# Kernel optimization log

Hardware: AMD Instinct MI355X
Metric: run time of the kernel (lower is better)

## Reference

```python
import jax, jax.numpy as jnp
import numpy as np

B, S, E, H, DH, W = 2, 4096, 1024, 16, 64, 512
NB = S // W          # number of query blocks
U = 2 * W            # key block = previous block + current block
INIT = 0.02


def setup_inputs() -> dict:
    key = jax.random.key(0)
    ks = jax.random.split(key, 6)
    x = jax.random.normal(ks[0], (B, S, E), jnp.float32)
    bias = jax.random.normal(ks[1], (H, W), jnp.float32)  # per-head alibi over rel. distance 0..W-1
    Wq = INIT * jax.random.normal(ks[2], (E, H, DH), jnp.float32)
    Wk = INIT * jax.random.normal(ks[3], (E, DH), jnp.float32)   # MQA: single shared K head
    Wv = INIT * jax.random.normal(ks[4], (E, DH), jnp.float32)   # MQA: single shared V head
    Wo = INIT * jax.random.normal(ks[5], (H, DH, E), jnp.float32)
    return {"x": x, "bias": bias, "Wq": Wq, "Wk": Wk, "Wv": Wv, "Wo": Wo}


def _sliding_window_attn(q, k, v, bias):
    # q: [B,S,H,DH]; k,v: [B,S,DH] (shared across heads); bias: [H,W]
    scale = 1.0 / np.sqrt(DH)
    qb = q.reshape(B, NB, W, H, DH)
    # pad one window of zeros in front so every query block sees a 'previous' block
    kp = jnp.pad(k, ((0, 0), (W, 0), (0, 0)))
    vp = jnp.pad(v, ((0, 0), (W, 0), (0, 0)))
    idx = jnp.arange(NB)[:, None] * W + jnp.arange(U)[None, :]  # [NB,U] into padded seq
    kb = kp[:, idx]  # [B,NB,U,DH]
    vb = vp[:, idx]  # [B,NB,U,DH]
    # scores over (query-in-block w, key-in-2W-block u)
    scores = jnp.einsum('bnwhd,bnud->bhnwu', qb, kb) * scale  # [B,H,NB,W,U]
    t = jnp.arange(W)
    u = jnp.arange(U)
    d = t[:, None] - u[None, :] + W                 # relative distance i-j, [W,U]
    rel_ok = (d >= 0) & (d < W)                     # causal + within window
    j_global = idx - W                              # global key position, [NB,U]
    valid = rel_ok[None, :, :] & (j_global >= 0)[:, None, :]  # [NB,W,U]
    bmat = bias[:, jnp.clip(d, 0, W - 1)]           # [H,W,U]
    scores = scores + bmat[None, :, None, :, :]
    neg = jnp.finfo(scores.dtype).min / 2
    scores = jnp.where(valid[None, None], scores, neg)
    p = jax.nn.softmax(scores, axis=-1)
    out = jnp.einsum('bhnwu,bnud->bnwhd', p, vb)    # [B,NB,W,H,DH]
    return out.reshape(B, S, H, DH)


def reference(x, bias, Wq, Wk, Wv, Wo):
    q = jnp.einsum('bse,ehd->bshd', x, Wq)
    k = jnp.einsum('bse,ed->bsd', x, Wk)
    v = jnp.einsum('bse,ed->bsd', x, Wv)
    attn = _sliding_window_attn(q, k, v, bias)
    return jnp.einsum('bshd,hde->bse', attn, Wo)
```

## Files before the change

### kernel.cpp

```cpp
#include <hip/hip_runtime.h>

#define Bx 2
#define Sx 4096
#define Ex 1024
#define Hx 16
#define DHx 64
#define Wwin 512

typedef unsigned short u16;
typedef __attribute__((ext_vector_type(8))) short bf16x8;
typedef __attribute__((ext_vector_type(4))) float f32x4;
typedef __attribute__((ext_vector_type(4))) unsigned short u16x4;

__device__ __forceinline__ u16 f2b(float f) {
  unsigned u = __builtin_bit_cast(unsigned, f);
  unsigned r = (u + 0x7FFFu + ((u >> 16) & 1u)) >> 16;
  return (u16)r;
}

__device__ __forceinline__ void gload_lds16(const void* g, void* l) {
  __builtin_amdgcn_global_load_lds(
      (const __attribute__((address_space(1))) void*)g,
      (__attribute__((address_space(3))) void*)l, 16, 0, 0);
}

__global__ __launch_bounds__(256) void cast_x_kernel(const float* __restrict__ x,
                                                     u16* __restrict__ xb) {
  long idx = ((long)blockIdx.x * 256 + threadIdx.x) * 4;
  float4 v = *(const float4*)(x + idx);
  u16x4 o;
  o[0] = f2b(v.x); o[1] = f2b(v.y); o[2] = f2b(v.z); o[3] = f2b(v.w);
  *(u16x4*)(xb + idx) = o;
}

__global__ __launch_bounds__(256) void pack_w_kernel(const float* __restrict__ Wq,
                                                     const float* __restrict__ Wk,
                                                     const float* __restrict__ Wv,
                                                     const float* __restrict__ Wo,
                                                     u16* __restrict__ wcat,
                                                     u16* __restrict__ wot) {
  int idx = blockIdx.x * 256 + threadIdx.x;
  if (idx < 1048576) {
    int e = idx >> 10, n = idx & 1023;
    wcat[n * 1024 + e] = f2b(Wq[idx]);
  } else if (idx < 1048576 + 65536) {
    int i2 = idx - 1048576;
    int e = i2 >> 6, d = i2 & 63;
    wcat[(1024 + d) * 1024 + e] = f2b(Wk[i2]);
  } else if (idx < 1048576 + 131072) {
    int i2 = idx - (1048576 + 65536);
    int e = i2 >> 6, d = i2 & 63;
    wcat[(1088 + d) * 1024 + e] = f2b(Wv[i2]);
  } else {
    int i2 = idx - (1048576 + 131072);
    int hd = i2 >> 10, e = i2 & 1023;
    wot[e * 1024 + hd] = f2b(Wo[i2]);
  }
}

template <typename OutT>
__global__ __launch_bounds__(256) void gemm_bt_kernel(const u16* __restrict__ A,
                                                      const u16* __restrict__ Bt,
                                                      OutT* __restrict__ C,
                                                      int M, int N, int K) {
  __shared__ u16 As[128 * 64];
  __shared__ u16 Bs[128 * 64];
  const int tid = threadIdx.x;
  const int lane = tid & 63, wave = tid >> 6;
  const int ll = lane & 15, gl = lane >> 4;
  const int wr = wave >> 1, wc = wave & 1;
  const long m0 = (long)blockIdx.x * 128;
  const long n0 = (long)blockIdx.y * 128;
  const int segrow = lane >> 3, cph = lane & 7;

  f32x4 acc[4][4] = {};

  for (int kb = 0; kb < K; kb += 64) {
    __syncthreads();
#pragma unroll
    for (int q = 0; q < 4; ++q) {
      int s = wave * 4 + q;
      int row = s * 8 + segrow;
      int clog = cph ^ (row & 7);
      gload_lds16(A + (m0 + row) * K + kb + clog * 8, (char*)As + s * 1024);
      gload_lds16(Bt + (n0 + row) * K + kb + clog * 8, (char*)Bs + s * 1024);
    }
    __syncthreads();
#pragma unroll
    for (int kx = 0; kx < 2; ++kx) {
      bf16x8 af[4], bfr[4];
#pragma unroll
      for (int rg = 0; rg < 4; ++rg) {
        int row = wr * 64 + rg * 16 + ll;
        int c = kx * 4 + gl;
        af[rg] = *(const bf16x8*)&As[row * 64 + ((c ^ (row & 7)) << 3)];
      }
#pragma unroll
      for (int cg = 0; cg < 4; ++cg) {
        int row = wc * 64 + cg * 16 + ll;
        int c = kx * 4 + gl;
        bfr[cg] = *(const bf16x8*)&Bs[row * 64 + ((c ^ (row & 7)) << 3)];
      }
#pragma unroll
      for (int rg = 0; rg < 4; ++rg)
#pragma unroll
        for (int cg = 0; cg < 4; ++cg)
          acc[rg][cg] = __builtin_amdgcn_mfma_f32_16x16x32_bf16(af[rg], bfr[cg],
                                                                acc[rg][cg], 0, 0, 0);
    }
  }
#pragma unroll
  for (int rg = 0; rg < 4; ++rg)
#pragma unroll
    for (int cg = 0; cg < 4; ++cg)
#pragma unroll
      for (int r = 0; r < 4; ++r) {
        long row = m0 + wr * 64 + rg * 16 + gl * 4 + r;
        long col = n0 + wc * 64 + cg * 16 + ll;
        if constexpr (sizeof(OutT) == 2)
          C[row * (long)N + col] = f2b(acc[rg][cg][r]);
        else
          C[row * (long)N + col] = acc[rg][cg][r];
      }
}

__global__ __launch_bounds__(256) void vt_transpose_kernel(const u16* __restrict__ qkvb,
                                                           u16* __restrict__ vt) {
  __shared__ u16 T[64 * 65];
  const int blk = blockIdx.x;
  const int b = blk >> 6;
  const int j0 = (blk & 63) * 64;
  const int tid = threadIdx.x;
#pragma unroll
  for (int rep = 0; rep < 16; ++rep) {
    int idx = rep * 256 + tid;
    int jj = idx >> 6, dd = idx & 63;
    T[dd * 65 + jj] = qkvb[((long)b * Sx + j0 + jj) * 1152 + 1088 + dd];
  }
  __syncthreads();
#pragma unroll
  for (int rep = 0; rep < 16; ++rep) {
    int idx = rep * 256 + tid;
    int dd = idx >> 6, jj = idx & 63;
    vt[((long)b * 64 + dd) * Sx + j0 + jj] = T[dd * 65 + jj];
  }
}

__global__ __launch_bounds__(256) void attn_kernel(const u16* __restrict__ qkv,
                                                   const u16* __restrict__ vt,
                                                   const float* __restrict__ bias,
                                                   u16* __restrict__ attnb) {
  __shared__ u16 Ks[64 * 64];
  __shared__ u16 Vts[64 * 64];
  __shared__ u16 Pb[4][32 * 64];
  __shared__ float biasS[512];

  const int bid = blockIdx.x;
  const int h = bid & 15;
  const int qt = (bid >> 4) & 31;
  const int b = bid >> 9;
  const int q0 = qt * 128;
  const long bS = (long)b * Sx;

  const int tid = threadIdx.x;
  const int lane = tid & 63, wave = tid >> 6;
  const int ll = lane & 15, gl = lane >> 4;
  const int wq0 = q0 + wave * 32;
  const int segrow = lane >> 3, cph = lane & 7;

  for (int i = tid; i < 512; i += 256) biasS[i] = bias[h * 512 + i];

  bf16x8 qf[2][2];
#pragma unroll
  for (int rg = 0; rg < 2; ++rg)
#pragma unroll
    for (int kx = 0; kx < 2; ++kx)
      qf[rg][kx] = *(const bf16x8*)&qkv[(bS + wq0 + rg * 16 + ll) * 1152 +
                                        h * 64 + kx * 32 + gl * 8];

  f32x4 oacc[2][4] = {};
  float mrow[2][4], lrow[2][4];
#pragma unroll
  for (int rg = 0; rg < 2; ++rg)
#pragma unroll
    for (int r = 0; r < 4; ++r) { mrow[rg][r] = -3e38f; lrow[rg][r] = 0.f; }

  u16* Pw = &Pb[wave][0];

  const int kb_start = (q0 - 512) > 0 ? (q0 - 512) : 0;
  const int kb_end = q0 + 64;
  for (int kb = kb_start; kb <= kb_end; kb += 64) {
#pragma unroll
    for (int q = 0; q < 2; ++q) {
      int s = wave * 2 + q;
      int rrow = s * 8 + segrow;
      int clog = cph ^ (rrow & 7);
      gload_lds16(qkv + (bS + kb + rrow) * 1152 + 1024 + clog * 8, (char*)Ks + s * 1024);
      gload_lds16(vt + ((long)b * 64 + rrow) * Sx + kb + clog * 8, (char*)Vts + s * 1024);
    }
    __syncthreads();
    const bool active = (kb <= wq0 + 31) && (kb + 63 >= wq0 - 511);
    if (active) {
      f32x4 sacc[2][4] = {};
#pragma unroll
      for (int kx = 0; kx < 2; ++kx) {
        bf16x8 kf[4];
#pragma unroll
        for (int cg = 0; cg < 4; ++cg) {
          int key = cg * 16 + ll;
          int c = kx * 4 + gl;
          kf[cg] = *(const bf16x8*)&Ks[key * 64 + ((c ^ (key & 7)) << 3)];
        }
#pragma unroll
        for (int rg = 0; rg < 2; ++rg)
#pragma unroll
          for (int cg = 0; cg < 4; ++cg)
            sacc[rg][cg] = __builtin_amdgcn_mfma_f32_16x16x32_bf16(qf[rg][kx], kf[cg],
                                                                   sacc[rg][cg], 0, 0, 0);
      }
#pragma unroll
      for (int rg = 0; rg < 2; ++rg) {
        float cmax[4] = {-3e38f, -3e38f, -3e38f, -3e38f};
#pragma unroll
        for (int cg = 0; cg < 4; ++cg)
#pragma unroll
          for (int r = 0; r < 4; ++r) {
            int i = wq0 + rg * 16 + gl * 4 + r;
            int j = kb + cg * 16 + ll;
            int d = i - j;
            int dc = d < 0 ? 0 : (d > 511 ? 511 : d);
            float sc = (d >= 0 && d < 512) ? fmaf(sacc[rg][cg][r], 0.125f, biasS[dc])
                                           : -1e30f;
            sacc[rg][cg][r] = sc;
            cmax[r] = fmaxf(cmax[r], sc);
          }
#pragma unroll
        for (int r = 0; r < 4; ++r) {
          cmax[r] = fmaxf(cmax[r], __shfl_xor(cmax[r], 1));
          cmax[r] = fmaxf(cmax[r], __shfl_xor(cmax[r], 2));
          cmax[r] = fmaxf(cmax[r], __shfl_xor(cmax[r], 4));
          cmax[r] = fmaxf(cmax[r], __shfl_xor(cmax[r], 8));
          float mnew = fmaxf(mrow[rg][r], cmax[r]);
          float f = __expf(mrow[rg][r] - mnew);
          mrow[rg][r] = mnew;
          lrow[rg][r] *= f;
#pragma unroll
          for (int cg = 0; cg < 4; ++cg) oacc[rg][cg][r] *= f;
        }
        float csum[4] = {0.f, 0.f, 0.f, 0.f};
#pragma unroll
        for (int cg = 0; cg < 4; ++cg)
#pragma unroll
          for (int r = 0; r < 4; ++r) {
            float p = __expf(sacc[rg][cg][r] - mrow[rg][r]);
            sacc[rg][cg][r] = p;
            csum[r] += p;
          }
#pragma unroll
        for (int r = 0; r < 4; ++r) {
          csum[r] += __shfl_xor(csum[r], 1);
          csum[r] += __shfl_xor(csum[r], 2);
          csum[r] += __shfl_xor(csum[r], 4);
          csum[r] += __shfl_xor(csum[r], 8);
          lrow[rg][r] += csum[r];
        }
#pragma unroll
        for (int cg = 0; cg < 4; ++cg)
#pragma unroll
          for (int r = 0; r < 4; ++r) {
            int row = rg * 16 + gl * 4 + r;
            int col = cg * 16 + ll;
            Pw[row * 64 + (((col >> 3) ^ (row & 7)) << 3) + (col & 7)] =
                f2b(sacc[rg][cg][r]);
          }
      }
#pragma unroll
      for (int kx = 0; kx < 2; ++kx) {
        bf16x8 pf[2], vf[4];
#pragma unroll
        for (int rg = 0; rg < 2; ++rg) {
          int row = rg * 16 + ll;
          int c = kx * 4 + gl;
          pf[rg] = *(const bf16x8*)&Pw[row * 64 + ((c ^ (row & 7)) << 3)];
        }
#pragma unroll
        for (int cg = 0; cg < 4; ++cg) {
          int dh = cg * 16 + ll;
          int c = kx * 4 + gl;
          vf[cg] = *(const bf16x8*)&Vts[dh * 64 + ((c ^ (dh & 7)) << 3)];
        }
#pragma unroll
        for (int rg = 0; rg < 2; ++rg)
#pragma unroll
          for (int cg = 0; cg < 4; ++cg)
            oacc[rg][cg] = __builtin_amdgcn_mfma_f32_16x16x32_bf16(pf[rg], vf[cg],
                                                                   oacc[rg][cg], 0, 0, 0);
      }
    }
    __syncthreads();
  }
#pragma unroll
  for (int rg = 0; rg < 2; ++rg)
#pragma unroll
    for (int r = 0; r < 4; ++r) {
      float inv = 1.0f / lrow[rg][r];
      long i = wq0 + rg * 16 + gl * 4 + r;
#pragma unroll
      for (int cg = 0; cg < 4; ++cg)
        attnb[(bS + i) * 1024 + h * 64 + cg * 16 + ll] = f2b(oacc[rg][cg][r] * inv);
    }
}

extern "C" void kernel_launch(void* const* d_in, const int* in_sizes, int n_in,
                              void* d_out, int out_size, void* d_ws, size_t ws_size,
                              hipStream_t stream) {
  const float* x    = (const float*)d_in[0];
  const float* bias = (const float*)d_in[1];
  const float* Wq   = (const float*)d_in[2];
  const float* Wk   = (const float*)d_in[3];
  const float* Wv   = (const float*)d_in[4];
  const float* Wo   = (const float*)d_in[5];
  float* out = (float*)d_out;

  u16* xb    = (u16*)d_ws;
  u16* wcat  = xb    + (size_t)8192 * 1024;
  u16* wot   = wcat  + (size_t)1152 * 1024;
  u16* qkvb  = wot   + (size_t)1024 * 1024;
  u16* vtb   = qkvb  + (size_t)8192 * 1152;
  u16* attnb = xb;

  cast_x_kernel<<<8192, 256, 0, stream>>>(x, xb);
  pack_w_kernel<<<8704, 256, 0, stream>>>(Wq, Wk, Wv, Wo, wcat, wot);
  gemm_bt_kernel<u16><<<dim3(64, 9), 256, 0, stream>>>(xb, wcat, qkvb, 8192, 1152, 1024);
  vt_transpose_kernel<<<128, 256, 0, stream>>>(qkvb, vtb);
  attn_kernel<<<1024, 256, 0, stream>>>(qkvb, vtb, bias, attnb);
  gemm_bt_kernel<float><<<dim3(64, 8), 256, 0, stream>>>(attnb, wot, out, 8192, 1024, 1024);
}
```

Measured before the change: 248.7 us.

## Drop online-softmax max tracking, load K/V directly per wave, compute row sums via MFMA

```diff
diff --git a/kernel.cpp b/kernel.cpp
--- a/kernel.cpp
+++ b/kernel.cpp
@@ -8,6 +8,7 @@
 #define Wwin 512
 
 typedef unsigned short u16;
+typedef unsigned int u32;
 typedef __attribute__((ext_vector_type(8))) short bf16x8;
 typedef __attribute__((ext_vector_type(4))) float f32x4;
 typedef __attribute__((ext_vector_type(4))) unsigned short u16x4;
@@ -16,6 +17,12 @@
   unsigned u = __builtin_bit_cast(unsigned, f);
   unsigned r = (u + 0x7FFFu + ((u >> 16) & 1u)) >> 16;
   return (u16)r;
+}
+
+__device__ __forceinline__ u32 cvt_pk_bf16(float lo, float hi) {
+  u32 r;
+  asm("v_cvt_pk_bf16_f32 %0, %1, %2" : "=v"(r) : "v"(lo), "v"(hi));
+  return r;
 }
 
 __device__ __forceinline__ void gload_lds16(const void* g, void* l) {
@@ -150,12 +157,11 @@
                                                    const u16* __restrict__ vt,
                                                    const float* __restrict__ bias,
                                                    u16* __restrict__ attnb) {
-  __shared__ u16 Ks[64 * 64];
-  __shared__ u16 Vts[64 * 64];
   __shared__ u16 Pb[4][32 * 64];
-  __shared__ float biasS[512];
-
-  const int bid = blockIdx.x;
+  __shared__ float bias2S[512];
+
+  const int bid0 = blockIdx.x;
+  const int bid = (bid0 & 7) * 128 + (bid0 >> 3);
   const int h = bid & 15;
   const int qt = (bid >> 4) & 31;
   const int b = bid >> 9;
@@ -166,9 +172,12 @@
   const int lane = tid & 63, wave = tid >> 6;
   const int ll = lane & 15, gl = lane >> 4;
   const int wq0 = q0 + wave * 32;
-  const int segrow = lane >> 3, cph = lane & 7;
-
-  for (int i = tid; i < 512; i += 256) biasS[i] = bias[h * 512 + i];
+
+  for (int i = tid; i < 512; i += 256)
+    bias2S[i] = fmaf(bias[h * 512 + i], 1.4426950408889634f, -24.0f);
+  __syncthreads();
+
+  const float C1 = 0.125f * 1.4426950408889634f;
 
   bf16x8 qf[2][2];
 #pragma unroll
@@ -178,132 +187,102 @@
       qf[rg][kx] = *(const bf16x8*)&qkv[(bS + wq0 + rg * 16 + ll) * 1152 +
                                         h * 64 + kx * 32 + gl * 8];
 
+  u16 ov = (ll == 0) ? (u16)0x3F80 : (u16)0;
+  bf16x8 vones;
+#pragma unroll
+  for (int i = 0; i < 8; ++i) vones[i] = (short)ov;
+
   f32x4 oacc[2][4] = {};
-  float mrow[2][4], lrow[2][4];
+  f32x4 lacc[2] = {};
+
+  u16* Pw = &Pb[wave][0];
+
+  const int kb_start = (wq0 > 511) ? ((wq0 - 511) & ~63) : 0;
+  const int kb_last = (wq0 + 31) & ~63;
+  for (int kb = kb_start; kb <= kb_last; kb += 64) {
+    bf16x8 kf[2][4], vfr[2][4];
+#pragma unroll
+    for (int kx = 0; kx < 2; ++kx)
+#pragma unroll
+      for (int cg = 0; cg < 4; ++cg) {
+        kf[kx][cg] = *(const bf16x8*)&qkv[(bS + kb + cg * 16 + ll) * 1152 + 1024 +
+                                          kx * 32 + gl * 8];
+        vfr[kx][cg] = *(const bf16x8*)&vt[((long)b * 64 + cg * 16 + ll) * Sx + kb +
+                                          kx * 32 + gl * 8];
+      }
+    f32x4 sacc[2][4] = {};
+#pragma unroll
+    for (int kx = 0; kx < 2; ++kx)
+#pragma unroll
+      for (int rg = 0; rg < 2; ++rg)
+#pragma unroll
+        for (int cg = 0; cg < 4; ++cg)
+          sacc[rg][cg] = __builtin_amdgcn_mfma_f32_16x16x32_bf16(qf[rg][kx], kf[kx][cg],
+                                                                 sacc[rg][cg], 0, 0, 0);
+    const int dbase = (wq0 - kb) + gl * 4 - ll;
+    const bool full = (kb - wq0 >= -480) && (kb - wq0 <= -64);
+    if (full) {
+      const float* bp = bias2S + dbase;
+#pragma unroll
+      for (int rg = 0; rg < 2; ++rg)
+#pragma unroll
+        for (int cg = 0; cg < 4; ++cg)
+#pragma unroll
+          for (int r = 0; r < 4; ++r)
+            sacc[rg][cg][r] =
+                __builtin_exp2f(fmaf(sacc[rg][cg][r], C1, bp[rg * 16 + r - cg * 16]));
+    } else {
+#pragma unroll
+      for (int rg = 0; rg < 2; ++rg)
+#pragma unroll
+        for (int cg = 0; cg < 4; ++cg)
+#pragma unroll
+          for (int r = 0; r < 4; ++r) {
+            int d = dbase + rg * 16 + r - cg * 16;
+            int dc = d < 0 ? 0 : (d > 511 ? 511 : d);
+            float p = __builtin_exp2f(fmaf(sacc[rg][cg][r], C1, bias2S[dc]));
+            sacc[rg][cg][r] = ((unsigned)d < 512u) ? p : 0.0f;
+          }
+    }
+#pragma unroll
+    for (int rg = 0; rg < 2; ++rg)
+#pragma unroll
+      for (int cg = 0; cg < 4; ++cg)
+#pragma unroll
+        for (int rp = 0; rp < 2; ++rp) {
+          u32 pk = cvt_pk_bf16(sacc[rg][cg][2 * rp], sacc[rg][cg][2 * rp + 1]);
+          int row0 = rg * 16 + gl * 4 + 2 * rp;
+          int col = cg * 16 + ll;
+          Pw[row0 * 64 + (((col >> 3) ^ (row0 & 7)) << 3) + (col & 7)] = (u16)pk;
+          int row1 = row0 + 1;
+          Pw[row1 * 64 + (((col >> 3) ^ (row1 & 7)) << 3) + (col & 7)] = (u16)(pk >> 16);
+        }
+#pragma unroll
+    for (int kx = 0; kx < 2; ++kx) {
+      bf16x8 pf[2];
+#pragma unroll
+      for (int rg = 0; rg < 2; ++rg) {
+        int row = rg * 16 + ll;
+        int c = kx * 4 + gl;
+        pf[rg] = *(const bf16x8*)&Pw[row * 64 + ((c ^ (row & 7)) << 3)];
+      }
+#pragma unroll
+      for (int rg = 0; rg < 2; ++rg) {
+#pragma unroll
+        for (int cg = 0; cg < 4; ++cg)
+          oacc[rg][cg] = __builtin_amdgcn_mfma_f32_16x16x32_bf16(pf[rg], vfr[kx][cg],
+                                                                 oacc[rg][cg], 0, 0, 0);
+        lacc[rg] = __builtin_amdgcn_mfma_f32_16x16x32_bf16(pf[rg], vones,
+                                                           lacc[rg], 0, 0, 0);
+      }
+    }
+  }
 #pragma unroll
   for (int rg = 0; rg < 2; ++rg)
 #pragma unroll
-    for (int r = 0; r < 4; ++r) { mrow[rg][r] = -3e38f; lrow[rg][r] = 0.f; }
-
-  u16* Pw = &Pb[wave][0];
-
-  const int kb_start = (q0 - 512) > 0 ? (q0 - 512) : 0;
-  const int kb_end = q0 + 64;
-  for (int kb = kb_start; kb <= kb_end; kb += 64) {
-#pragma unroll
-    for (int q = 0; q < 2; ++q) {
-      int s = wave * 2 + q;
-      int rrow = s * 8 + segrow;
-      int clog = cph ^ (rrow & 7);
-      gload_lds16(qkv + (bS + kb + rrow) * 1152 + 1024 + clog * 8, (char*)Ks + s * 1024);
-      gload_lds16(vt + ((long)b * 64 + rrow) * Sx + kb + clog * 8, (char*)Vts + s * 1024);
-    }
-    __syncthreads();
-    const bool active = (kb <= wq0 + 31) && (kb + 63 >= wq0 - 511);
-    if (active) {
-      f32x4 sacc[2][4] = {};
-#pragma unroll
-      for (int kx = 0; kx < 2; ++kx) {
-        bf16x8 kf[4];
-#pragma unroll
-        for (int cg = 0; cg < 4; ++cg) {
-          int key = cg * 16 + ll;
-          int c = kx * 4 + gl;
-          kf[cg] = *(const bf16x8*)&Ks[key * 64 + ((c ^ (key & 7)) << 3)];
-        }
-#pragma unroll
-        for (int rg = 0; rg < 2; ++rg)
-#pragma unroll
-          for (int cg = 0; cg < 4; ++cg)
-            sacc[rg][cg] = __builtin_amdgcn_mfma_f32_16x16x32_bf16(qf[rg][kx], kf[cg],
-                                                                   sacc[rg][cg], 0, 0, 0);
-      }
-#pragma unroll
-      for (int rg = 0; rg < 2; ++rg) {
-        float cmax[4] = {-3e38f, -3e38f, -3e38f, -3e38f};
-#pragma unroll
-        for (int cg = 0; cg < 4; ++cg)
-#pragma unroll
-          for (int r = 0; r < 4; ++r) {
-            int i = wq0 + rg * 16 + gl * 4 + r;
-            int j = kb + cg * 16 + ll;
-            int d = i - j;
-            int dc = d < 0 ? 0 : (d > 511 ? 511 : d);
-            float sc = (d >= 0 && d < 512) ? fmaf(sacc[rg][cg][r], 0.125f, biasS[dc])
-                                           : -1e30f;
-            sacc[rg][cg][r] = sc;
-            cmax[r] = fmaxf(cmax[r], sc);
-          }
-#pragma unroll
-        for (int r = 0; r < 4; ++r) {
-          cmax[r] = fmaxf(cmax[r], __shfl_xor(cmax[r], 1));
-          cmax[r] = fmaxf(cmax[r], __shfl_xor(cmax[r], 2));
-          cmax[r] = fmaxf(cmax[r], __shfl_xor(cmax[r], 4));
-          cmax[r] = fmaxf(cmax[r], __shfl_xor(cmax[r], 8));
-          float mnew = fmaxf(mrow[rg][r], cmax[r]);
-          float f = __expf(mrow[rg][r] - mnew);
-          mrow[rg][r] = mnew;
-          lrow[rg][r] *= f;
-#pragma unroll
-          for (int cg = 0; cg < 4; ++cg) oacc[rg][cg][r] *= f;
-        }
-        float csum[4] = {0.f, 0.f, 0.f, 0.f};
-#pragma unroll
-        for (int cg = 0; cg < 4; ++cg)
-#pragma unroll
-          for (int r = 0; r < 4; ++r) {
-            float p = __expf(sacc[rg][cg][r] - mrow[rg][r]);
-            sacc[rg][cg][r] = p;
-            csum[r] += p;
-          }
-#pragma unroll
-        for (int r = 0; r < 4; ++r) {
-          csum[r] += __shfl_xor(csum[r], 1);
-          csum[r] += __shfl_xor(csum[r], 2);
-          csum[r] += __shfl_xor(csum[r], 4);
-          csum[r] += __shfl_xor(csum[r], 8);
-          lrow[rg][r] += csum[r];
-        }
-#pragma unroll
-        for (int cg = 0; cg < 4; ++cg)
-#pragma unroll
-          for (int r = 0; r < 4; ++r) {
-            int row = rg * 16 + gl * 4 + r;
-            int col = cg * 16 + ll;
-            Pw[row * 64 + (((col >> 3) ^ (row & 7)) << 3) + (col & 7)] =
-                f2b(sacc[rg][cg][r]);
-          }
-      }
-#pragma unroll
-      for (int kx = 0; kx < 2; ++kx) {
-        bf16x8 pf[2], vf[4];
-#pragma unroll
-        for (int rg = 0; rg < 2; ++rg) {
-          int row = rg * 16 + ll;
-          int c = kx * 4 + gl;
-          pf[rg] = *(const bf16x8*)&Pw[row * 64 + ((c ^ (row & 7)) << 3)];
-        }
-#pragma unroll
-        for (int cg = 0; cg < 4; ++cg) {
-          int dh = cg * 16 + ll;
-          int c = kx * 4 + gl;
-          vf[cg] = *(const bf16x8*)&Vts[dh * 64 + ((c ^ (dh & 7)) << 3)];
-        }
-#pragma unroll
-        for (int rg = 0; rg < 2; ++rg)
-#pragma unroll
-          for (int cg = 0; cg < 4; ++cg)
-            oacc[rg][cg] = __builtin_amdgcn_mfma_f32_16x16x32_bf16(pf[rg], vf[cg],
-                                                                   oacc[rg][cg], 0, 0, 0);
-      }
-    }
-    __syncthreads();
-  }
-#pragma unroll
-  for (int rg = 0; rg < 2; ++rg)
-#pragma unroll
     for (int r = 0; r < 4; ++r) {
-      float inv = 1.0f / lrow[rg][r];
+      float l = __shfl(lacc[rg][r], lane & 48);
+      float inv = 1.0f / l;
       long i = wq0 + rg * 16 + gl * 4 + r;
 #pragma unroll
       for (int cg = 0; cg < 4; ++cg)
```

After: 231.0 us. 7.1% less time.
